# Kernel tuning notes

Hardware: AMD Instinct MI355X
Metric: run time of the kernel (lower is better)

## Reference

```python
import jax, jax.numpy as jnp
import numpy as np

MUL = 64            # channel multiplicity per l
B = 8               # number of systems (equal-size MOLE segments)
N = 64000           # total edges
E = 8               # experts
OFFS = (0, 1, 4)    # per-l offsets inside D_total=9 rotation matrix
DTOT = 9
DIM = MUL * DTOT    # 1152

# ---- z-rotation scatter pattern (build_z_rot_multi): diag=cos(f*ang), antidiag=sin(f*ang), f = l - i ----
_rows, _anti, _freq = [], [], []
for l, off in zip(range(3), OFFS):
    for i in range(2 * l + 1):
        _rows.append(off + i); _anti.append(off + 2 * l - i); _freq.append(l - i)
_rows = np.array(_rows); _anti = np.array(_anti)
ROWS = jnp.array(_rows); FREQ = jnp.array(np.array(_freq, dtype=np.float32))
_nc = _rows != _anti  # exclude diag/antidiag overlap (center) from sin scatter
ROWS_NC = jnp.array(_rows[_nc]); ANTI_NC = jnp.array(_anti[_nc]); NCJ = jnp.array(np.where(_nc)[0])

# ---- per-m gather/scatter index tables (m_in_mask/m_out_mask) for irreps 64x0e+64x1o+64x2e ----
_c = np.arange(MUL)
M0_IDX = jnp.array(np.concatenate([_c, 64 + 3 * _c + 1, 256 + 5 * _c + 2]))                 # [192] centers
M1_IDX = jnp.array(np.stack([np.concatenate([64 + 3 * _c, 256 + 5 * _c + 1]),
                             np.concatenate([64 + 3 * _c + 2, 256 + 5 * _c + 3])], 1))      # [128,2] (-m,+m)
M2_IDX = jnp.array(np.stack([256 + 5 * _c, 256 + 5 * _c + 4], 1))                            # [64,2]


def _z_rot(angles):
    # scatter cos/sin into dense [N,9,9] block-diagonal z-rotation (irregular-access hot spot)
    c = jnp.cos(angles[:, None] * FREQ[None, :])
    s = jnp.sin(angles[:, None] * FREQ[None, :])
    X = jnp.zeros((angles.shape[0], DTOT, DTOT), angles.dtype)
    X = X.at[:, ROWS, ROWS].set(c)
    X = X.at[:, ROWS_NC, ANTI_NC].set(s[:, NCJ])
    return X


def _wigner(alpha, beta, gamma, Jf):
    Xa, Xb, Xc = _z_rot(alpha), _z_rot(beta), _z_rot(gamma)
    return Xa @ Jf @ Xb @ Jf @ Xc  # [N,9,9]


def _rotate(x, D):
    # apply block-diagonal Wigner D per l-block of each channel
    parts, col = [], 0
    for l, off in zip(range(3), OFFS):
        d = 2 * l + 1
        xl = x[:, col:col + MUL * d].reshape(-1, MUL, d)
        Dl = D[:, off:off + d, off:off + d]
        parts.append(jnp.einsum('nij,ncj->nci', Dl, xl).reshape(-1, MUL * d))
        col += MUL * d
    return jnp.concatenate(parts, axis=1)


def _mole(x, coef, We, Ws, be=None, bs=None):
    # MOLELinear: per-system expert-mixed weights + shared expert; equal-size segments
    W = jnp.einsum('be,eoi->boi', coef, We) + Ws[None]
    y = jnp.einsum('bti,boi->bto', x.reshape(B, -1, x.shape[-1]), W)
    if be is not None:
        y = y + (jnp.einsum('be,eo->bo', coef, be) + bs)[:, None, :]
    return y.reshape(x.shape[:-1] + (W.shape[1],))


def setup_inputs() -> dict:
    key = jax.random.key(0)
    ks = jax.random.split(key, 16)
    k0 = 1.0 / np.sqrt(192.0); k1 = 1.0 / np.sqrt(128.0 * 2.0); k2 = 1.0 / np.sqrt(64.0 * 2.0)
    two_pi = 6.2831853
    return dict(
        x=jax.random.normal(ks[0], (N, DIM), jnp.float32),
        alpha=jax.random.uniform(ks[1], (N,), jnp.float32, 0.0, two_pi),
        beta=jax.random.uniform(ks[2], (N,), jnp.float32, 0.0, two_pi),
        gamma=jax.random.uniform(ks[3], (N,), jnp.float32, 0.0, two_pi),
        coefficients=jax.nn.softmax(jax.random.normal(ks[4], (B, E), jnp.float32), axis=-1),
        Jd1=jax.random.normal(ks[5], (3, 3), jnp.float32),
        Jd2=jax.random.normal(ks[6], (5, 5), jnp.float32),
        w_m0=jax.random.normal(ks[7], (E, 192, 192), jnp.float32) * k0,
        b_m0=jax.random.normal(ks[8], (E, 192), jnp.float32) * k0,
        ws_m0=jax.random.normal(ks[9], (192, 192), jnp.float32) * k0,
        bs_m0=jax.random.normal(ks[10], (192,), jnp.float32) * k0,
        w_m1=jax.random.normal(ks[11], (E, 256, 128), jnp.float32) * k1,
        ws_m1=jax.random.normal(ks[12], (256, 128), jnp.float32) * k1,
        w_m2=jax.random.normal(ks[13], (E, 128, 64), jnp.float32) * k2,
        ws_m2=jax.random.normal(ks[14], (128, 64), jnp.float32) * k2,
    )


def reference(x, alpha, beta, gamma, coefficients, Jd1, Jd2,
              w_m0, b_m0, ws_m0, bs_m0, w_m1, ws_m1, w_m2, ws_m2):
    # block-diagonal J (Jd constants per l)
    Jf = (jnp.zeros((DTOT, DTOT), x.dtype)
          .at[0, 0].set(1.0)
          .at[1:4, 1:4].set(Jd1)
          .at[4:9, 4:9].set(Jd2))
    # rotate_in
    xr = _rotate(x, _wigner(alpha, beta, gamma, Jf))
    out = jnp.zeros((x.shape[0], DIM), x.dtype)
    # m = 0 path (MOLE linear with bias)
    out = out.at[:, M0_IDX].set(_mole(xr[:, M0_IDX], coefficients, w_m0, ws_m0, b_m0, bs_m0))
    # m > 0 paths (SO2_m_Linear, no bias)
    for IDX, We, Ws in ((M1_IDX, w_m1, ws_m1), (M2_IDX, w_m2, ws_m2)):
        C_out = We.shape[1] // 2
        xg = xr[:, IDX.reshape(-1)].reshape(-1, IDX.shape[0], 2).transpose(0, 2, 1)  # [N,2,C] rows=(-m,+m)
        y = _mole(xg, coefficients, We, Ws)                                            # [N,2,2*C_out]
        y_r, y_i = y[..., :C_out], y[..., C_out:]
        om = y_r[:, 0] - y_i[:, 1]
        op = y_r[:, 1] + y_i[:, 0]
        out = out.at[:, IDX.reshape(-1)].set(jnp.stack([om, op], -1).reshape(-1, 2 * C_out))
    # rotate_out (inverse rotation)
    out = _rotate(out, _wigner(-gamma, -beta, -alpha, Jf))
    return out
```

## Files before the change

kernel.cpp:

```cpp
#include <hip/hip_runtime.h>
#include <cstddef>

#define NS 64000
#define GROUP 8000
#define TM 64

typedef __bf16 bf16x8 __attribute__((ext_vector_type(8)));
typedef float floatx4 __attribute__((ext_vector_type(4)));
typedef unsigned short ushort_t;

static const size_t BY_W0 = 0;
static const size_t BY_W1 = BY_W0 + 589824;
static const size_t BY_W2 = BY_W1 + 1048576;
static const size_t BY_B0 = BY_W2 + 262144;

__device__ __forceinline__ unsigned short f2bf(float f) {
    unsigned u = __float_as_uint(f);
    u += 0x7fff + ((u >> 16) & 1);
    return (unsigned short)(u >> 16);
}

__global__ __launch_bounds__(256) void mix_kernel(
    const float* __restrict__ coef,
    const float* __restrict__ w_m0, const float* __restrict__ b_m0,
    const float* __restrict__ ws_m0, const float* __restrict__ bs_m0,
    const float* __restrict__ w_m1, const float* __restrict__ ws_m1,
    const float* __restrict__ w_m2, const float* __restrict__ ws_m2,
    ushort_t* __restrict__ W0, float* __restrict__ B0,
    ushort_t* __restrict__ W1, ushort_t* __restrict__ W2)
{
    int tid = blockIdx.x * 256 + threadIdx.x;
    if (tid < 294912) {
        int b = tid / 36864, rem = tid % 36864;
        float s = ws_m0[rem];
        #pragma unroll
        for (int e = 0; e < 8; e++) s += coef[b * 8 + e] * w_m0[e * 36864 + rem];
        W0[tid] = f2bf(s);
    } else if (tid < 296448) {
        int i2 = tid - 294912;
        int b = i2 / 192, o = i2 % 192;
        float s = bs_m0[o];
        #pragma unroll
        for (int e = 0; e < 8; e++) s += coef[b * 8 + e] * b_m0[e * 192 + o];
        B0[i2] = s;
    } else if (tid < 820736) {
        int i3 = tid - 296448;
        int b = i3 >> 16, rem = i3 & 65535;
        int o = rem >> 8, i = rem & 255;
        int r, cc; float sign = 1.0f;
        if (o < 128) { if (i < 128) { r = o;       cc = i; } else { r = 128 + o;      cc = i - 128; sign = -1.0f; } }
        else { int o2 = o - 128; if (i < 128) { r = 128 + o2; cc = i; } else { r = o2; cc = i - 128; } }
        int idx = r * 128 + cc;
        float s = ws_m1[idx];
        #pragma unroll
        for (int e = 0; e < 8; e++) s += coef[b * 8 + e] * w_m1[e * 32768 + idx];
        W1[i3] = f2bf(sign * s);
    } else if (tid < 951808) {
        int i4 = tid - 820736;
        int b = i4 >> 14, rem = i4 & 16383;
        int o = rem >> 7, i = rem & 127;
        int r, cc; float sign = 1.0f;
        if (o < 64) { if (i < 64) { r = o;      cc = i; } else { r = 64 + o;      cc = i - 64; sign = -1.0f; } }
        else { int o2 = o - 64; if (i < 64) { r = 64 + o2; cc = i; } else { r = o2; cc = i - 64; } }
        int idx = r * 64 + cc;
        float s = ws_m2[idx];
        #pragma unroll
        for (int e = 0; e < 8; e++) s += coef[b * 8 + e] * w_m2[e * 8192 + idx];
        W2[i4] = f2bf(sign * s);
    }
}

__device__ __forceinline__ void zrot1(float& v0, float& v2, float c, float s) {
    float t0 = c * v0 + s * v2;
    v2 = -s * v0 + c * v2;
    v0 = t0;
}
__device__ __forceinline__ void j1mul(const float* J, float& v0, float& v1, float& v2) {
    float w0 = J[0] * v0 + J[1] * v1 + J[2] * v2;
    float w1 = J[3] * v0 + J[4] * v1 + J[5] * v2;
    float w2 = J[6] * v0 + J[7] * v1 + J[8] * v2;
    v0 = w0; v1 = w1; v2 = w2;
}
__device__ __forceinline__ void zrot2(float& u0, float& u1, float& u3, float& u4,
                                      float c1, float s1, float c2, float s2) {
    float t0 = c2 * u0 + s2 * u4;
    u4 = -s2 * u0 + c2 * u4;
    u0 = t0;
    float t1 = c1 * u1 + s1 * u3;
    u3 = -s1 * u1 + c1 * u3;
    u1 = t1;
}
__device__ __forceinline__ void j2mul(const float* J, float& u0, float& u1, float& u2, float& u3, float& u4) {
    float w0 = J[0]  * u0 + J[1]  * u1 + J[2]  * u2 + J[3]  * u3 + J[4]  * u4;
    float w1 = J[5]  * u0 + J[6]  * u1 + J[7]  * u2 + J[8]  * u3 + J[9]  * u4;
    float w2 = J[10] * u0 + J[11] * u1 + J[12] * u2 + J[13] * u3 + J[14] * u4;
    float w3 = J[15] * u0 + J[16] * u1 + J[17] * u2 + J[18] * u3 + J[19] * u4;
    float w4 = J[20] * u0 + J[21] * u1 + J[22] * u2 + J[23] * u3 + J[24] * u4;
    u0 = w0; u1 = w1; u2 = w2; u3 = w3; u4 = w4;
}

__device__ __forceinline__ int sidx(int row, int k, int K) {
    int gr = (k >> 3) ^ (row & 7);
    return row * K + gr * 8 + (k & 7);
}
__device__ __forceinline__ float yread(const ushort_t* L, int row, int k, int K) {
    unsigned u = L[sidx(row, k, K)];
    return __uint_as_float(u << 16);
}

template<int K, int NT>
__device__ __forceinline__ void gemm_seg(
    floatx4 (*acc)[4],
    const ushort_t* __restrict__ Wseg,
    const ushort_t* XL_,
    int mi, int quad)
{
    #pragma unroll
    for (int k0 = 0; k0 < K; k0 += 32) {
        bf16x8 af[4];
        #pragma unroll
        for (int ms = 0; ms < 4; ms++) {
            int row = ms * 16 + mi;
            int gr = ((k0 >> 3) + quad) ^ (row & 7);
            af[ms] = *(const bf16x8*)&XL_[row * K + gr * 8];
        }
        bf16x8 bfr[NT];
        #pragma unroll
        for (int t = 0; t < NT; t++)
            bfr[t] = *(const bf16x8*)&Wseg[(size_t)(t * 16 + mi) * K + k0 + quad * 8];
        #pragma unroll
        for (int t = 0; t < NT; t++)
            #pragma unroll
            for (int ms = 0; ms < 4; ms++)
                acc[t][ms] = __builtin_amdgcn_mfma_f32_16x16x32_bf16(af[ms], bfr[t], acc[t][ms], 0, 0, 0);
    }
}

template<int K, int NT, bool BIAS>
__device__ __forceinline__ void ywrite(
    floatx4 (*acc)[4], ushort_t* L, int n0, const float* __restrict__ bias,
    int mi, int quad)
{
    #pragma unroll
    for (int t = 0; t < NT; t++) {
        int col = n0 + t * 16 + mi;
        float bv = BIAS ? bias[col] : 0.f;
        int gc = col >> 3, kw = col & 7;
        #pragma unroll
        for (int ms = 0; ms < 4; ms++) {
            #pragma unroll
            for (int r = 0; r < 4; r++) {
                int m = ms * 16 + quad * 4 + r;
                L[m * K + ((gc ^ (m & 7)) * 8) + kw] = f2bf(acc[t][ms][r] + bv);
            }
        }
    }
}

__global__ __launch_bounds__(256, 2) void fused_kernel(
    const float* __restrict__ x,
    const float* __restrict__ alpha, const float* __restrict__ beta, const float* __restrict__ gamma_,
    const float* __restrict__ Jd1, const float* __restrict__ Jd2,
    const ushort_t* __restrict__ W0, const ushort_t* __restrict__ W1, const ushort_t* __restrict__ W2,
    const float* __restrict__ B0,
    float* __restrict__ out)
{
    __shared__ ushort_t XL[36864];
    __shared__ float TR[64 * 6];
    __shared__ float JL[34];

    ushort_t* X0L = XL;
    ushort_t* X1L = XL + 12288;
    ushort_t* X2L = XL + 28672;

    int t = threadIdx.x;
    int w = t >> 6, lane = t & 63;
    int g = blockIdx.x / 125;
    int base = g * GROUP + (blockIdx.x % 125) * TM;

    if (t < 64) {
        int n = base + t;
        float sa, ca, sb, cb, sg, cg;
        __sincosf(alpha[n],  &sa, &ca);
        __sincosf(beta[n],   &sb, &cb);
        __sincosf(gamma_[n], &sg, &cg);
        TR[t * 6 + 0] = sa; TR[t * 6 + 1] = ca;
        TR[t * 6 + 2] = sb; TR[t * 6 + 3] = cb;
        TR[t * 6 + 4] = sg; TR[t * 6 + 5] = cg;
    } else if (t < 98) {
        int j = t - 64;
        JL[j] = (j < 9) ? Jd1[j] : Jd2[j - 9];
    }
    __syncthreads();

    const float* J1 = JL;
    const float* J2 = JL + 9;
    int c = lane;

    for (int i = 0; i < 16; i++) {
        int nl = w * 16 + i;
        const float* xr = x + (size_t)(base + nl) * 576;
        float sa = TR[nl * 6 + 0], ca = TR[nl * 6 + 1];
        float sb = TR[nl * 6 + 2], cb = TR[nl * 6 + 3];
        float sg = TR[nl * 6 + 4], cg = TR[nl * 6 + 5];
        float s2a = 2.f * sa * ca, c2a = ca * ca - sa * sa;
        float s2b = 2.f * sb * cb, c2b = cb * cb - sb * sb;
        float s2g = 2.f * sg * cg, c2g = cg * cg - sg * sg;

        float v0 = xr[64 + 3 * c], v1 = xr[64 + 3 * c + 1], v2 = xr[64 + 3 * c + 2];
        zrot1(v0, v2, cg, sg);
        j1mul(J1, v0, v1, v2);
        zrot1(v0, v2, cb, sb);
        j1mul(J1, v0, v1, v2);
        zrot1(v0, v2, ca, sa);

        float u0 = xr[256 + 5 * c], u1 = xr[256 + 5 * c + 1], u2 = xr[256 + 5 * c + 2],
              u3 = xr[256 + 5 * c + 3], u4 = xr[256 + 5 * c + 4];
        zrot2(u0, u1, u3, u4, cg, sg, c2g, s2g);
        j2mul(J2, u0, u1, u2, u3, u4);
        zrot2(u0, u1, u3, u4, cb, sb, c2b, s2b);
        j2mul(J2, u0, u1, u2, u3, u4);
        zrot2(u0, u1, u3, u4, ca, sa, c2a, s2a);

        X0L[sidx(nl, c, 192)]       = f2bf(xr[c]);
        X0L[sidx(nl, 64 + c, 192)]  = f2bf(v1);
        X0L[sidx(nl, 128 + c, 192)] = f2bf(u2);
        X1L[sidx(nl, c, 256)]       = f2bf(v0);
        X1L[sidx(nl, 64 + c, 256)]  = f2bf(u1);
        X1L[sidx(nl, 128 + c, 256)] = f2bf(v2);
        X1L[sidx(nl, 192 + c, 256)] = f2bf(u3);
        X2L[sidx(nl, c, 128)]       = f2bf(u0);
        X2L[sidx(nl, 64 + c, 128)]  = f2bf(u4);
    }
    __syncthreads();

    int mi = lane & 15, quad = lane >> 4;
    floatx4 acc[10][4];
    #pragma unroll
    for (int a = 0; a < 10; a++)
        #pragma unroll
        for (int b2 = 0; b2 < 4; b2++) acc[a][b2] = (floatx4)0.f;

    const ushort_t* W0g = W0 + (size_t)g * 192 * 192;
    const ushort_t* W1g = W1 + (size_t)g * 256 * 256;
    const ushort_t* W2g = W2 + (size_t)g * 128 * 128;

    if (w == 0) {
        gemm_seg<192, 10>(acc, W0g, X0L, mi, quad);
    } else if (w == 1) {
        gemm_seg<256, 8>(acc, W1g, X1L, mi, quad);
    } else if (w == 2) {
        gemm_seg<256, 8>(acc, W1g + (size_t)128 * 256, X1L, mi, quad);
    } else {
        gemm_seg<192, 2>(acc, W0g + (size_t)160 * 192, X0L, mi, quad);
        gemm_seg<128, 8>(acc + 2, W2g, X2L, mi, quad);
    }

    __syncthreads();

    const float* B0g = B0 + g * 192;
    if (w == 0) {
        ywrite<192, 10, true>(acc, X0L, 0, B0g, mi, quad);
    } else if (w == 1) {
        ywrite<256, 8, false>(acc, X1L, 0, nullptr, mi, quad);
    } else if (w == 2) {
        ywrite<256, 8, false>(acc, X1L, 128, nullptr, mi, quad);
    } else {
        ywrite<192, 2, true>(acc, X0L, 160, B0g, mi, quad);
        ywrite<128, 8, false>(acc + 2, X2L, 0, nullptr, mi, quad);
    }
    __syncthreads();

    for (int i = 0; i < 16; i++) {
        int nl = w * 16 + i;
        float sa = -TR[nl * 6 + 0], ca = TR[nl * 6 + 1];
        float sb = -TR[nl * 6 + 2], cb = TR[nl * 6 + 3];
        float sg = -TR[nl * 6 + 4], cg = TR[nl * 6 + 5];
        float s2a = 2.f * sa * ca, c2a = ca * ca - sa * sa;
        float s2b = 2.f * sb * cb, c2b = cb * cb - sb * sb;
        float s2g = 2.f * sg * cg, c2g = cg * cg - sg * sg;

        float* orow = out + (size_t)(base + nl) * 576;

        orow[c] = yread(X0L, nl, c, 192);

        float v0 = yread(X1L, nl, c, 256);
        float v1 = yread(X0L, nl, 64 + c, 192);
        float v2 = yread(X1L, nl, 128 + c, 256);
        zrot1(v0, v2, ca, sa);
        j1mul(J1, v0, v1, v2);
        zrot1(v0, v2, cb, sb);
        j1mul(J1, v0, v1, v2);
        zrot1(v0, v2, cg, sg);
        orow[64 + 3 * c]     = v0;
        orow[64 + 3 * c + 1] = v1;
        orow[64 + 3 * c + 2] = v2;

        float u0 = yread(X2L, nl, c, 128);
        float u1 = yread(X1L, nl, 64 + c, 256);
        float u2 = yread(X0L, nl, 128 + c, 192);
        float u3 = yread(X1L, nl, 192 + c, 256);
        float u4 = yread(X2L, nl, 64 + c, 128);
        zrot2(u0, u1, u3, u4, ca, sa, c2a, s2a);
        j2mul(J2, u0, u1, u2, u3, u4);
        zrot2(u0, u1, u3, u4, cb, sb, c2b, s2b);
        j2mul(J2, u0, u1, u2, u3, u4);
        zrot2(u0, u1, u3, u4, cg, sg, c2g, s2g);
        orow[256 + 5 * c]     = u0;
        orow[256 + 5 * c + 1] = u1;
        orow[256 + 5 * c + 2] = u2;
        orow[256 + 5 * c + 3] = u3;
        orow[256 + 5 * c + 4] = u4;
    }
}

extern "C" void kernel_launch(void* const* d_in, const int* in_sizes, int n_in,
                              void* d_out, int out_size, void* d_ws, size_t ws_size,
                              hipStream_t stream)
{
    const float* x      = (const float*)d_in[0];
    const float* alpha  = (const float*)d_in[1];
    const float* beta   = (const float*)d_in[2];
    const float* gamma_ = (const float*)d_in[3];
    const float* coef   = (const float*)d_in[4];
    const float* Jd1    = (const float*)d_in[5];
    const float* Jd2    = (const float*)d_in[6];
    const float* w_m0   = (const float*)d_in[7];
    const float* b_m0   = (const float*)d_in[8];
    const float* ws_m0  = (const float*)d_in[9];
    const float* bs_m0  = (const float*)d_in[10];
    const float* w_m1   = (const float*)d_in[11];
    const float* ws_m1  = (const float*)d_in[12];
    const float* w_m2   = (const float*)d_in[13];
    const float* ws_m2  = (const float*)d_in[14];

    char* wsb = (char*)d_ws;
    ushort_t* W0 = (ushort_t*)(wsb + BY_W0);
    ushort_t* W1 = (ushort_t*)(wsb + BY_W1);
    ushort_t* W2 = (ushort_t*)(wsb + BY_W2);
    float*    B0 = (float*)(wsb + BY_B0);
    float*    out = (float*)d_out;

    hipLaunchKernelGGL(mix_kernel, dim3(3718), dim3(256), 0, stream,
                       coef, w_m0, b_m0, ws_m0, bs_m0, w_m1, ws_m1, w_m2, ws_m2,
                       W0, B0, W1, W2);
    hipLaunchKernelGGL(fused_kernel, dim3(1000), dim3(256), 0, stream,
                       x, alpha, beta, gamma_, Jd1, Jd2, W0, W1, W2, B0, out);
}
```

Measured before the change: 335.7 us.

## Use 512-thread blocks, split GEMM rows across wave halves, prefetch x rows

The fused kernel moves from 4 to 8 waves per block. Each wave handles 8 edges instead of 16 in the rotate phases, and in the GEMM phase the row tile is split so each wave computes 32 rows with half the accumulators. The rotate-in loop now double-buffers global loads of the next edge's row, and B-fragments are loaded per tile inside the MFMA loop. The aim is more waves per CU to hide memory latency and lower register pressure, at the cost of every weight fragment being read twice per block (once per row half).

```diff
diff --git a/kernel.cpp b/kernel.cpp
--- a/kernel.cpp
+++ b/kernel.cpp
@@ -108,38 +108,43 @@
     return __uint_as_float(u << 16);
 }
 
+__device__ __forceinline__ void load_row(const float* __restrict__ x, int n, int c, float* v) {
+    const float* xr = x + (size_t)n * 576;
+    v[0] = xr[c];
+    v[1] = xr[64 + 3 * c];  v[2] = xr[64 + 3 * c + 1];  v[3] = xr[64 + 3 * c + 2];
+    v[4] = xr[256 + 5 * c]; v[5] = xr[256 + 5 * c + 1]; v[6] = xr[256 + 5 * c + 2];
+    v[7] = xr[256 + 5 * c + 3]; v[8] = xr[256 + 5 * c + 4];
+}
+
 template<int K, int NT>
 __device__ __forceinline__ void gemm_seg(
-    floatx4 (*acc)[4],
+    floatx4 (*acc)[2],
     const ushort_t* __restrict__ Wseg,
     const ushort_t* XL_,
-    int mi, int quad)
+    int mi, int quad, int mh)
 {
     #pragma unroll
     for (int k0 = 0; k0 < K; k0 += 32) {
-        bf16x8 af[4];
-        #pragma unroll
-        for (int ms = 0; ms < 4; ms++) {
-            int row = ms * 16 + mi;
+        bf16x8 af[2];
+        #pragma unroll
+        for (int ms = 0; ms < 2; ms++) {
+            int row = mh * 32 + ms * 16 + mi;
             int gr = ((k0 >> 3) + quad) ^ (row & 7);
             af[ms] = *(const bf16x8*)&XL_[row * K + gr * 8];
         }
-        bf16x8 bfr[NT];
-        #pragma unroll
-        for (int t = 0; t < NT; t++)
-            bfr[t] = *(const bf16x8*)&Wseg[(size_t)(t * 16 + mi) * K + k0 + quad * 8];
-        #pragma unroll
-        for (int t = 0; t < NT; t++)
-            #pragma unroll
-            for (int ms = 0; ms < 4; ms++)
-                acc[t][ms] = __builtin_amdgcn_mfma_f32_16x16x32_bf16(af[ms], bfr[t], acc[t][ms], 0, 0, 0);
+        #pragma unroll
+        for (int t = 0; t < NT; t++) {
+            bf16x8 bt = *(const bf16x8*)&Wseg[(size_t)(t * 16 + mi) * K + k0 + quad * 8];
+            acc[t][0] = __builtin_amdgcn_mfma_f32_16x16x32_bf16(af[0], bt, acc[t][0], 0, 0, 0);
+            acc[t][1] = __builtin_amdgcn_mfma_f32_16x16x32_bf16(af[1], bt, acc[t][1], 0, 0, 0);
+        }
     }
 }
 
 template<int K, int NT, bool BIAS>
 __device__ __forceinline__ void ywrite(
-    floatx4 (*acc)[4], ushort_t* L, int n0, const float* __restrict__ bias,
-    int mi, int quad)
+    floatx4 (*acc)[2], ushort_t* L, int n0, const float* __restrict__ bias,
+    int mi, int quad, int mh)
 {
     #pragma unroll
     for (int t = 0; t < NT; t++) {
@@ -147,17 +152,17 @@
         float bv = BIAS ? bias[col] : 0.f;
         int gc = col >> 3, kw = col & 7;
         #pragma unroll
-        for (int ms = 0; ms < 4; ms++) {
+        for (int ms = 0; ms < 2; ms++) {
             #pragma unroll
             for (int r = 0; r < 4; r++) {
-                int m = ms * 16 + quad * 4 + r;
+                int m = mh * 32 + ms * 16 + quad * 4 + r;
                 L[m * K + ((gc ^ (m & 7)) * 8) + kw] = f2bf(acc[t][ms][r] + bv);
             }
         }
     }
 }
 
-__global__ __launch_bounds__(256, 2) void fused_kernel(
+__global__ __launch_bounds__(512, 4) void fused_kernel(
     const float* __restrict__ x,
     const float* __restrict__ alpha, const float* __restrict__ beta, const float* __restrict__ gamma_,
     const float* __restrict__ Jd1, const float* __restrict__ Jd2,
@@ -197,82 +202,90 @@
     const float* J2 = JL + 9;
     int c = lane;
 
-    for (int i = 0; i < 16; i++) {
-        int nl = w * 16 + i;
-        const float* xr = x + (size_t)(base + nl) * 576;
-        float sa = TR[nl * 6 + 0], ca = TR[nl * 6 + 1];
-        float sb = TR[nl * 6 + 2], cb = TR[nl * 6 + 3];
-        float sg = TR[nl * 6 + 4], cg = TR[nl * 6 + 5];
-        float s2a = 2.f * sa * ca, c2a = ca * ca - sa * sa;
-        float s2b = 2.f * sb * cb, c2b = cb * cb - sb * sb;
-        float s2g = 2.f * sg * cg, c2g = cg * cg - sg * sg;
-
-        float v0 = xr[64 + 3 * c], v1 = xr[64 + 3 * c + 1], v2 = xr[64 + 3 * c + 2];
-        zrot1(v0, v2, cg, sg);
-        j1mul(J1, v0, v1, v2);
-        zrot1(v0, v2, cb, sb);
-        j1mul(J1, v0, v1, v2);
-        zrot1(v0, v2, ca, sa);
-
-        float u0 = xr[256 + 5 * c], u1 = xr[256 + 5 * c + 1], u2 = xr[256 + 5 * c + 2],
-              u3 = xr[256 + 5 * c + 3], u4 = xr[256 + 5 * c + 4];
-        zrot2(u0, u1, u3, u4, cg, sg, c2g, s2g);
-        j2mul(J2, u0, u1, u2, u3, u4);
-        zrot2(u0, u1, u3, u4, cb, sb, c2b, s2b);
-        j2mul(J2, u0, u1, u2, u3, u4);
-        zrot2(u0, u1, u3, u4, ca, sa, c2a, s2a);
-
-        X0L[sidx(nl, c, 192)]       = f2bf(xr[c]);
-        X0L[sidx(nl, 64 + c, 192)]  = f2bf(v1);
-        X0L[sidx(nl, 128 + c, 192)] = f2bf(u2);
-        X1L[sidx(nl, c, 256)]       = f2bf(v0);
-        X1L[sidx(nl, 64 + c, 256)]  = f2bf(u1);
-        X1L[sidx(nl, 128 + c, 256)] = f2bf(v2);
-        X1L[sidx(nl, 192 + c, 256)] = f2bf(u3);
-        X2L[sidx(nl, c, 128)]       = f2bf(u0);
-        X2L[sidx(nl, 64 + c, 128)]  = f2bf(u4);
+    {
+        float va[9], vb[9];
+        load_row(x, base + w * 8, c, va);
+        #pragma unroll
+        for (int i = 0; i < 8; i++) {
+            float* cu = (i & 1) ? vb : va;
+            float* nx = (i & 1) ? va : vb;
+            if (i < 7) load_row(x, base + w * 8 + i + 1, c, nx);
+
+            int nl = w * 8 + i;
+            float sa = TR[nl * 6 + 0], ca = TR[nl * 6 + 1];
+            float sb = TR[nl * 6 + 2], cb = TR[nl * 6 + 3];
+            float sg = TR[nl * 6 + 4], cg = TR[nl * 6 + 5];
+            float s2a = 2.f * sa * ca, c2a = ca * ca - sa * sa;
+            float s2b = 2.f * sb * cb, c2b = cb * cb - sb * sb;
+            float s2g = 2.f * sg * cg, c2g = cg * cg - sg * sg;
+
+            float v0 = cu[1], v1 = cu[2], v2 = cu[3];
+            zrot1(v0, v2, cg, sg);
+            j1mul(J1, v0, v1, v2);
+            zrot1(v0, v2, cb, sb);
+            j1mul(J1, v0, v1, v2);
+            zrot1(v0, v2, ca, sa);
+
+            float u0 = cu[4], u1 = cu[5], u2 = cu[6], u3 = cu[7], u4 = cu[8];
+            zrot2(u0, u1, u3, u4, cg, sg, c2g, s2g);
+            j2mul(J2, u0, u1, u2, u3, u4);
+            zrot2(u0, u1, u3, u4, cb, sb, c2b, s2b);
+            j2mul(J2, u0, u1, u2, u3, u4);
+            zrot2(u0, u1, u3, u4, ca, sa, c2a, s2a);
+
+            X0L[sidx(nl, c, 192)]       = f2bf(cu[0]);
+            X0L[sidx(nl, 64 + c, 192)]  = f2bf(v1);
+            X0L[sidx(nl, 128 + c, 192)] = f2bf(u2);
+            X1L[sidx(nl, c, 256)]       = f2bf(v0);
+            X1L[sidx(nl, 64 + c, 256)]  = f2bf(u1);
+            X1L[sidx(nl, 128 + c, 256)] = f2bf(v2);
+            X1L[sidx(nl, 192 + c, 256)] = f2bf(u3);
+            X2L[sidx(nl, c, 128)]       = f2bf(u0);
+            X2L[sidx(nl, 64 + c, 128)]  = f2bf(u4);
+        }
     }
     __syncthreads();
 
     int mi = lane & 15, quad = lane >> 4;
-    floatx4 acc[10][4];
+    int cg = w & 3, mh = w >> 2;
+    floatx4 acc[10][2];
     #pragma unroll
     for (int a = 0; a < 10; a++)
         #pragma unroll
-        for (int b2 = 0; b2 < 4; b2++) acc[a][b2] = (floatx4)0.f;
+        for (int b2 = 0; b2 < 2; b2++) acc[a][b2] = (floatx4)0.f;
 
     const ushort_t* W0g = W0 + (size_t)g * 192 * 192;
     const ushort_t* W1g = W1 + (size_t)g * 256 * 256;
     const ushort_t* W2g = W2 + (size_t)g * 128 * 128;
 
-    if (w == 0) {
-        gemm_seg<192, 10>(acc, W0g, X0L, mi, quad);
-    } else if (w == 1) {
-        gemm_seg<256, 8>(acc, W1g, X1L, mi, quad);
-    } else if (w == 2) {
-        gemm_seg<256, 8>(acc, W1g + (size_t)128 * 256, X1L, mi, quad);
+    if (cg == 0) {
+        gemm_seg<192, 10>(acc, W0g, X0L, mi, quad, mh);
+    } else if (cg == 1) {
+        gemm_seg<256, 8>(acc, W1g, X1L, mi, quad, mh);
+    } else if (cg == 2) {
+        gemm_seg<256, 8>(acc, W1g + (size_t)128 * 256, X1L, mi, quad, mh);
     } else {
-        gemm_seg<192, 2>(acc, W0g + (size_t)160 * 192, X0L, mi, quad);
-        gemm_seg<128, 8>(acc + 2, W2g, X2L, mi, quad);
+        gemm_seg<192, 2>(acc, W0g + (size_t)160 * 192, X0L, mi, quad, mh);
+        gemm_seg<128, 8>(acc + 2, W2g, X2L, mi, quad, mh);
     }
 
     __syncthreads();
 
     const float* B0g = B0 + g * 192;
-    if (w == 0) {
-        ywrite<192, 10, true>(acc, X0L, 0, B0g, mi, quad);
-    } else if (w == 1) {
-        ywrite<256, 8, false>(acc, X1L, 0, nullptr, mi, quad);
-    } else if (w == 2) {
-        ywrite<256, 8, false>(acc, X1L, 128, nullptr, mi, quad);
+    if (cg == 0) {
+        ywrite<192, 10, true>(acc, X0L, 0, B0g, mi, quad, mh);
+    } else if (cg == 1) {
+        ywrite<256, 8, false>(acc, X1L, 0, nullptr, mi, quad, mh);
+    } else if (cg == 2) {
+        ywrite<256, 8, false>(acc, X1L, 128, nullptr, mi, quad, mh);
     } else {
-        ywrite<192, 2, true>(acc, X0L, 160, B0g, mi, quad);
-        ywrite<128, 8, false>(acc + 2, X2L, 0, nullptr, mi, quad);
+        ywrite<192, 2, true>(acc, X0L, 160, B0g, mi, quad, mh);
+        ywrite<128, 8, false>(acc + 2, X2L, 0, nullptr, mi, quad, mh);
     }
     __syncthreads();
 
-    for (int i = 0; i < 16; i++) {
-        int nl = w * 16 + i;
+    for (int i = 0; i < 8; i++) {
+        int nl = w * 8 + i;
         float sa = -TR[nl * 6 + 0], ca = TR[nl * 6 + 1];
         float sb = -TR[nl * 6 + 2], cb = TR[nl * 6 + 3];
         float sg = -TR[nl * 6 + 4], cg = TR[nl * 6 + 5];
@@ -344,6 +357,6 @@
     hipLaunchKernelGGL(mix_kernel, dim3(3718), dim3(256), 0, stream,
                        coef, w_m0, b_m0, ws_m0, bs_m0, w_m1, ws_m1, w_m2, ws_m2,
                        W0, B0, W1, W2);
-    hipLaunchKernelGGL(fused_kernel, dim3(1000), dim3(256), 0, stream,
+    hipLaunchKernelGGL(fused_kernel, dim3(1000), dim3(512), 0, stream,
                        x, alpha, beta, gamma_, Jd1, Jd2, W0, W1, W2, B0, out);
 }
```

After: 352.7 us. 5.0% more time.
